# Kernel tuning notes

Measured on AMD Instinct MI355X. Metric: run time of the kernel, lower is better.

The kernel has to match this reference:

```python
import jax, jax.numpy as jnp
import numpy as np

N_TRUCK = 100000
N_CAR = 100000
E = 1600000
H = 128
P = 200000


def _gcn(x, edge_index, edge_weight, W, b, num_nodes):
    """PyG GCNConv: D^{-1/2}(A+I)D^{-1/2} x W + b with self-loop weight 1."""
    h = x @ W  # [N, H]
    row, col = edge_index[0], edge_index[1]
    deg = jax.ops.segment_sum(edge_weight, col, num_segments=num_nodes) + 1.0  # +1 self-loop
    dis = jax.lax.rsqrt(deg)
    norm = dis[row] * edge_weight * dis[col]  # [E]
    agg = jax.ops.segment_sum(norm[:, None] * h[row], col, num_segments=num_nodes)
    agg = agg + (dis * dis)[:, None] * h  # self-loop contribution
    return agg + b


def setup_inputs() -> dict:
    key = jax.random.key(0)
    ks = jax.random.split(key, 12)
    return {
        "x_car": jax.random.normal(ks[0], (N_CAR, 3), dtype=jnp.float32),
        "edge_index_truck": jax.random.randint(ks[1], (2, E), 0, N_TRUCK, dtype=jnp.int64)
        if jax.config.jax_enable_x64 else jax.random.randint(ks[1], (2, E), 0, N_TRUCK, dtype=jnp.int32),
        "edge_index_car": jax.random.randint(ks[2], (2, E), 0, N_CAR, dtype=jnp.int32),
        "edge_weight_car": jax.random.uniform(ks[3], (E,), dtype=jnp.float32),
        "src": jax.random.randint(ks[4], (P,), 0, N_TRUCK + N_CAR, dtype=jnp.int32),
        "dst": jax.random.randint(ks[5], (P,), 0, N_TRUCK + N_CAR, dtype=jnp.int32),
        "n_truck": N_TRUCK,
        "W_truck": jax.random.normal(ks[6], (1, H), dtype=jnp.float32) * 0.5,
        "b_truck": jax.random.normal(ks[7], (H,), dtype=jnp.float32) * 0.1,
        "W_car": jax.random.normal(ks[8], (3, H), dtype=jnp.float32) * 0.5,
        "b_car": jax.random.normal(ks[9], (H,), dtype=jnp.float32) * 0.1,
        "W_lin": jax.random.normal(ks[10], (H, 1), dtype=jnp.float32) * 0.1,
        "b_lin": jax.random.normal(ks[11], (1,), dtype=jnp.float32) * 0.1,
    }


def reference(x_car, edge_index_truck, edge_index_car, edge_weight_car,
              src, dst, n_truck, W_truck, b_truck, W_car, b_car, W_lin, b_lin):
    x_truck_in = jnp.ones((n_truck, 1), dtype=x_car.dtype)
    ew_truck = jnp.ones((edge_index_truck.shape[1],), dtype=x_car.dtype)
    h_truck = _gcn(x_truck_in, edge_index_truck, ew_truck, W_truck, b_truck, n_truck)
    h_car = _gcn(x_car, edge_index_car, edge_weight_car, W_car, b_car, x_car.shape[0])
    x = jnp.concatenate([h_truck, h_car], axis=0)  # [N_truck+N_car, H]
    score = (x[src] * x[dst]) @ W_lin + b_lin  # [P, 1]
    return score
```

## Files before the change

### kernel.cpp

```cpp
#include <hip/hip_runtime.h>

typedef unsigned long long u64;

#define N_TRUCK 100000
#define BLK 256
#define NB 256
#define NPB 391
#define CAP 8192
#define PB 512
#define BLK_PL 512
#define BLK_P 1024
#define CHUNK_MAX 3136
#define ROW_MASK 0x1FFFFu
#define LC_SHIFT 17

#define WS_NEED_NEW 29569920ULL


__global__ __launch_bounds__(BLK_PL, 8)
void k_place(const int* __restrict__ trow, const int* __restrict__ tcol,
             const int* __restrict__ crow, const int* __restrict__ ccol,
             const float* __restrict__ ew, int E_,
             int* __restrict__ curT, int* __restrict__ curC,
             unsigned* __restrict__ pT, u64* __restrict__ pC8,
             const float* __restrict__ Wt, const float* __restrict__ bt,
             const float* __restrict__ Wc, const float* __restrict__ bc,
             const float* __restrict__ wlin, float* __restrict__ G) {
    if (blockIdx.x == PB) {
        int l = threadIdx.x;
        if (l < 64) {
            float acc[21];
#pragma unroll
            for (int k = 0; k < 21; k++) acc[k] = 0.0f;
            for (int h = l; h < 128; h += 64) {
                float m[6] = {Wt[h], bt[h], Wc[h], Wc[128 + h], Wc[256 + h], bc[h]};
                float w = wlin[h];
                int k = 0;
#pragma unroll
                for (int a = 0; a < 6; a++)
#pragma unroll
                    for (int b2 = a; b2 < 6; b2++)
                        acc[k++] += m[a] * m[b2] * w;
            }
            int k = 0;
#pragma unroll
            for (int a = 0; a < 6; a++)
#pragma unroll
                for (int b2 = a; b2 < 6; b2++) {
                    float v = acc[k++];
#pragma unroll
                    for (int off = 32; off; off >>= 1) v += __shfl_down(v, off);
                    if (l == 0) {
                        G[a * 6 + b2] = v;
                        G[b2 * 6 + a] = v;
                    }
                }
        }
        return;
    }

    __shared__ u64 pay8[CHUNK_MAX];
    __shared__ unsigned char bkt[CHUNK_MAX];
    __shared__ int hT[NB], hC[NB];
    __shared__ int shiftA[NB];
    __shared__ int wsum[8];
    unsigned* pay4 = (unsigned*)pay8;

    const int b = blockIdx.x;
    const int t = threadIdx.x;
    const int lane = t & 63, wv = t >> 6;
    const int chunk = (E_ + PB - 1) / PB;
    const int s0 = b * chunk, s1 = min(E_, s0 + chunk);
    const int n = s1 - s0;

    for (int k = t; k < NB; k += BLK_PL) { hT[k] = 0; hC[k] = 0; }
    __syncthreads();
    for (int j = s0 + t; j < s1; j += BLK_PL) {
        int tc = tcol[j];
        int cc = ccol[j];
        atomicAdd(&hT[tc / NPB], 1);
        atomicAdd(&hC[cc / NPB], 1);
    }
    __syncthreads();

    {
        int cntk = 0, inc = 0;
        if (t < NB) {
            cntk = hT[t];
            inc = cntk;
#pragma unroll
            for (int off = 1; off < 64; off <<= 1) {
                int nv = __shfl_up(inc, off);
                if (lane >= off) inc += nv;
            }
            if (lane == 63) wsum[wv] = inc;
        }
        __syncthreads();
        if (t < 4) {
            int pv = wsum[t], pinc = pv;
#pragma unroll
            for (int off = 1; off < 4; off <<= 1) {
                int nv = __shfl_up(pinc, off);
                if (lane >= off) pinc += nv;
            }
            wsum[t] = pinc - pv;
        }
        __syncthreads();
        if (t < NB) {
            int lexcl = (inc - cntk) + wsum[wv];
            int gstart = t * CAP + atomicAdd(&curT[t], cntk);
            hT[t] = lexcl;
            shiftA[t] = gstart - lexcl;
        }
        __syncthreads();
        for (int j = s0 + t; j < s1; j += BLK_PL) {
            int tc = tcol[j];
            int k = tc / NPB;
            int s = atomicAdd(&hT[k], 1);
            pay4[s] = ((unsigned)(tc - k * NPB) << LC_SHIFT) | (unsigned)trow[j];
            bkt[s] = (unsigned char)k;
        }
        __syncthreads();
        for (int s = t; s < n; s += BLK_PL)
            pT[s + shiftA[bkt[s]]] = pay4[s];
        __syncthreads();
    }

    {
        int cntk = 0, inc = 0;
        if (t < NB) {
            cntk = hC[t];
            inc = cntk;
#pragma unroll
            for (int off = 1; off < 64; off <<= 1) {
                int nv = __shfl_up(inc, off);
                if (lane >= off) inc += nv;
            }
            if (lane == 63) wsum[wv] = inc;
        }
        __syncthreads();
        if (t < 4) {
            int pv = wsum[t], pinc = pv;
#pragma unroll
            for (int off = 1; off < 4; off <<= 1) {
                int nv = __shfl_up(pinc, off);
                if (lane >= off) pinc += nv;
            }
            wsum[t] = pinc - pv;
        }
        __syncthreads();
        if (t < NB) {
            int lexcl = (inc - cntk) + wsum[wv];
            int gstart = t * CAP + atomicAdd(&curC[t], cntk);
            hC[t] = lexcl;
            shiftA[t] = gstart - lexcl;
        }
        __syncthreads();
        for (int j = s0 + t; j < s1; j += BLK_PL) {
            int cc = ccol[j];
            int k = cc / NPB;
            int s = atomicAdd(&hC[k], 1);
            unsigned lo = ((unsigned)(cc - k * NPB) << LC_SHIFT) | (unsigned)crow[j];
            pay8[s] = ((u64)__float_as_uint(ew[j]) << 32) | lo;
            bkt[s] = (unsigned char)k;
        }
        __syncthreads();
        for (int s = t; s < n; s += BLK_PL)
            pC8[s + shiftA[bkt[s]]] = pay8[s];
    }
}


__global__ void k_deg2(const unsigned* __restrict__ pT, const u64* __restrict__ pC8,
                       const int* __restrict__ curT, const int* __restrict__ curC,
                       const float* __restrict__ x_car,
                       float* __restrict__ dis_t, float* __restrict__ dis_c,
                       float4* __restrict__ xs4, int nt, int nc) {
    __shared__ float acc[NPB];
    int b = blockIdx.x;
    bool car = b >= NB;
    int bk = car ? b - NB : b;
    int cnt = car ? curC[bk] : curT[bk];
    int s0 = bk * CAP;
    for (int k = threadIdx.x; k < NPB; k += blockDim.x) acc[k] = 0.0f;
    __syncthreads();
    if (car) {
        const ulonglong2* p2 = (const ulonglong2*)(pC8 + s0);
        int half = cnt >> 1;
        for (int j = threadIdx.x; j < half; j += blockDim.x) {
            ulonglong2 v = p2[j];
            atomicAdd(&acc[((unsigned)v.x) >> LC_SHIFT], __uint_as_float((unsigned)(v.x >> 32)));
            atomicAdd(&acc[((unsigned)v.y) >> LC_SHIFT], __uint_as_float((unsigned)(v.y >> 32)));
        }
        if ((cnt & 1) && threadIdx.x == 0) {
            u64 v = pC8[s0 + cnt - 1];
            atomicAdd(&acc[((unsigned)v) >> LC_SHIFT], __uint_as_float((unsigned)(v >> 32)));
        }
    } else {
        const uint2* p2 = (const uint2*)(pT + s0);
        int half = cnt >> 1;
        for (int j = threadIdx.x; j < half; j += blockDim.x) {
            uint2 v = p2[j];
            atomicAdd(&acc[v.x >> LC_SHIFT], 1.0f);
            atomicAdd(&acc[v.y >> LC_SHIFT], 1.0f);
        }
        if ((cnt & 1) && threadIdx.x == 0)
            atomicAdd(&acc[pT[s0 + cnt - 1] >> LC_SHIFT], 1.0f);
    }
    __syncthreads();
    int ntot = car ? nc : nt;
    for (int nn = threadIdx.x; nn < NPB; nn += blockDim.x) {
        int node = bk * NPB + nn;
        if (node < ntot) {
            float d = rsqrtf(acc[nn] + 1.0f);
            if (car) {
                dis_c[node] = d;
                const float* xn = &x_car[3 * node];
                xs4[node] = make_float4(d * xn[0], d * xn[1], d * xn[2], d);
            } else {
                dis_t[node] = d;
            }
        }
    }
}


__global__ void k_agg(const unsigned* __restrict__ pT, const u64* __restrict__ pC8,
                      const int* __restrict__ curT, const int* __restrict__ curC,
                      const float* __restrict__ dis_t, const float* __restrict__ dis_c,
                      const float4* __restrict__ xs4,
                      float* __restrict__ s_t, float4* __restrict__ y4,
                      int nt, int nc) {
    int b = blockIdx.x;
    if (b < NB) {
        __shared__ float sacc[NPB];
        int cnt = curT[b];
        int s0 = b * CAP;
        for (int k = threadIdx.x; k < NPB; k += blockDim.x) sacc[k] = 0.0f;
        __syncthreads();
        const uint2* p2 = (const uint2*)(pT + s0);
        int half = cnt >> 1;
        for (int j = threadIdx.x; j < half; j += blockDim.x) {
            uint2 v = p2[j];
            float da = dis_t[v.x & ROW_MASK];
            float db = dis_t[v.y & ROW_MASK];
            atomicAdd(&sacc[v.x >> LC_SHIFT], da);
            atomicAdd(&sacc[v.y >> LC_SHIFT], db);
        }
        if ((cnt & 1) && threadIdx.x == 0) {
            unsigned v = pT[s0 + cnt - 1];
            atomicAdd(&sacc[v >> LC_SHIFT], dis_t[v & ROW_MASK]);
        }
        __syncthreads();
        for (int nn = threadIdx.x; nn < NPB; nn += blockDim.x) {
            int node = b * NPB + nn;
            if (node < nt) {
                float d = dis_t[node];
                s_t[node] = fmaf(d, sacc[nn], d * d);
            }
        }
    } else {
        int bk = b - NB;
        __shared__ float y[NPB * 5];
        __shared__ float dcl[NPB];
        int cnt = curC[bk];
        int s0 = bk * CAP;
        for (int k = threadIdx.x; k < NPB * 5; k += blockDim.x) y[k] = 0.0f;
        for (int k = threadIdx.x; k < NPB; k += blockDim.x) {
            int node = bk * NPB + k;
            dcl[k] = (node < nc) ? dis_c[node] : 0.0f;
        }
        __syncthreads();
        const ulonglong2* p2 = (const ulonglong2*)(pC8 + s0);
        int half = cnt >> 1;
        for (int j = threadIdx.x; j < half; j += blockDim.x) {
            ulonglong2 v = p2[j];
            unsigned loa = (unsigned)v.x, lob = (unsigned)v.y;
            float4 xa = xs4[loa & ROW_MASK];
            float4 xb = xs4[lob & ROW_MASK];
            int lca = loa >> LC_SHIFT, lcb = lob >> LC_SHIFT;
            float na = __uint_as_float((unsigned)(v.x >> 32)) * dcl[lca];
            float nb = __uint_as_float((unsigned)(v.y >> 32)) * dcl[lcb];
            atomicAdd(&y[lca * 5 + 0], na * xa.x);
            atomicAdd(&y[lca * 5 + 1], na * xa.y);
            atomicAdd(&y[lca * 5 + 2], na * xa.z);
            atomicAdd(&y[lcb * 5 + 0], nb * xb.x);
            atomicAdd(&y[lcb * 5 + 1], nb * xb.y);
            atomicAdd(&y[lcb * 5 + 2], nb * xb.z);
        }
        if ((cnt & 1) && threadIdx.x == 0) {
            u64 v = pC8[s0 + cnt - 1];
            unsigned lo = (unsigned)v;
            float4 xa = xs4[lo & ROW_MASK];
            int lc = lo >> LC_SHIFT;
            float na = __uint_as_float((unsigned)(v >> 32)) * dcl[lc];
            atomicAdd(&y[lc * 5 + 0], na * xa.x);
            atomicAdd(&y[lc * 5 + 1], na * xa.y);
            atomicAdd(&y[lc * 5 + 2], na * xa.z);
        }
        __syncthreads();
        for (int nn = threadIdx.x; nn < NPB; nn += blockDim.x) {
            int node = bk * NPB + nn;
            if (node < nc) {
                float d = dcl[nn];
                float4 xs = xs4[node];
                y4[node] = make_float4(fmaf(d, xs.x, y[nn * 5 + 0]),
                                       fmaf(d, xs.y, y[nn * 5 + 1]),
                                       fmaf(d, xs.z, y[nn * 5 + 2]), 1.0f);
            }
        }
    }
}


__device__ __forceinline__ void load_zf(int i, const float* __restrict__ s_t,
                                        const float4* __restrict__ y4, float z[6]) {
    if (i < N_TRUCK) {
        z[0] = s_t[i]; z[1] = 1.0f; z[2] = 0.0f; z[3] = 0.0f; z[4] = 0.0f; z[5] = 0.0f;
    } else {
        float4 y = y4[i - N_TRUCK];
        z[0] = 0.0f; z[1] = 0.0f; z[2] = y.x; z[3] = y.y; z[4] = y.z; z[5] = 1.0f;
    }
}

__global__ void k_pairs(const int* __restrict__ src, const int* __restrict__ dst, int P_,
                        const float* __restrict__ s_t, const float4* __restrict__ y4,
                        const float* __restrict__ G, const float* __restrict__ b_lin,
                        float* __restrict__ out) {
    int p = blockIdx.x * blockDim.x + threadIdx.x;
    if (p >= P_) return;
    float zs[6], zd[6];
    load_zf(src[p], s_t, y4, zs);
    load_zf(dst[p], s_t, y4, zd);
    float acc = 0.0f;
#pragma unroll
    for (int a = 0; a < 6; a++) {
        float g = 0.0f;
#pragma unroll
        for (int b = 0; b < 6; b++) g = fmaf(G[a * 6 + b], zd[b], g);
        acc = fmaf(zs[a], g, acc);
    }
    out[p] = acc + b_lin[0];
}


__global__ void k_G(const float* __restrict__ Wt, const float* __restrict__ bt,
                    const float* __restrict__ Wc, const float* __restrict__ bc,
                    const float* __restrict__ wlin, float* __restrict__ G) {
    int l = threadIdx.x;
    float acc[21];
#pragma unroll
    for (int k = 0; k < 21; k++) acc[k] = 0.0f;
    for (int h = l; h < 128; h += 64) {
        float m[6] = {Wt[h], bt[h], Wc[h], Wc[128 + h], Wc[256 + h], bc[h]};
        float w = wlin[h];
        int k = 0;
#pragma unroll
        for (int a = 0; a < 6; a++)
#pragma unroll
            for (int b = a; b < 6; b++)
                acc[k++] += m[a] * m[b] * w;
    }
    int k = 0;
#pragma unroll
    for (int a = 0; a < 6; a++)
#pragma unroll
        for (int b = a; b < 6; b++) {
            float v = acc[k++];
#pragma unroll
            for (int off = 32; off; off >>= 1) v += __shfl_down(v, off);
            if (l == 0) {
                G[a * 6 + b] = v;
                G[b * 6 + a] = v;
            }
        }
}

__global__ void k_deg(const int* __restrict__ tcol, const int* __restrict__ ccol,
                      const float* __restrict__ ew, int E_,
                      int* __restrict__ cnt_t, float* __restrict__ degw_c) {
    int i = blockIdx.x * blockDim.x + threadIdx.x;
    if (i >= E_) return;
    atomicAdd(&cnt_t[tcol[i]], 1);
    atomicAdd(&degw_c[ccol[i]], ew[i]);
}

__global__ void k_dis(const int* __restrict__ cnt_t, const float* __restrict__ degw_c,
                      float* __restrict__ dis_t, float* __restrict__ dis_c,
                      int nt, int nc) {
    int i = blockIdx.x * blockDim.x + threadIdx.x;
    if (i < nt) dis_t[i] = rsqrtf((float)cnt_t[i] + 1.0f);
    if (i < nc) dis_c[i] = rsqrtf(degw_c[i] + 1.0f);
}

__global__ void k_scat(const int* __restrict__ trow, const int* __restrict__ tcol,
                       const int* __restrict__ crow, const int* __restrict__ ccol,
                       const float* __restrict__ ew, int E_,
                       const float* __restrict__ dis_t, const float* __restrict__ dis_c,
                       const float* __restrict__ x_car,
                       float* __restrict__ sumdis, float* __restrict__ y4) {
    int i = blockIdx.x * blockDim.x + threadIdx.x;
    if (i >= E_) return;
    atomicAdd(&sumdis[tcol[i]], dis_t[trow[i]]);
    int r = crow[i], c = ccol[i];
    float nrm = dis_c[r] * ew[i] * dis_c[c];
    atomicAdd(&y4[c * 4 + 0], nrm * x_car[r * 3 + 0]);
    atomicAdd(&y4[c * 4 + 1], nrm * x_car[r * 3 + 1]);
    atomicAdd(&y4[c * 4 + 2], nrm * x_car[r * 3 + 2]);
}

__global__ void k_fin(int nt, int nc,
                      const float* __restrict__ dis_t, const float* __restrict__ sumdis,
                      float* __restrict__ s_t,
                      const float* __restrict__ dis_c, const float* __restrict__ x_car,
                      float* __restrict__ y4) {
    int i = blockIdx.x * blockDim.x + threadIdx.x;
    if (i < nt) {
        float d = dis_t[i];
        s_t[i] = d * sumdis[i] + d * d;
    }
    if (i < nc) {
        float d2 = dis_c[i] * dis_c[i];
        y4[i * 4 + 0] += d2 * x_car[i * 3 + 0];
        y4[i * 4 + 1] += d2 * x_car[i * 3 + 1];
        y4[i * 4 + 2] += d2 * x_car[i * 3 + 2];
        y4[i * 4 + 3] = 1.0f;
    }
}


extern "C" void kernel_launch(void* const* d_in, const int* in_sizes, int n_in,
                              void* d_out, int out_size, void* d_ws, size_t ws_size,
                              hipStream_t stream) {
    const float* x_car  = (const float*)d_in[0];
    const int*   ei_t   = (const int*)d_in[1];
    const int*   ei_c   = (const int*)d_in[2];
    const float* ew_c   = (const float*)d_in[3];
    const int*   src    = (const int*)d_in[4];
    const int*   dst    = (const int*)d_in[5];
    const float* W_t    = (const float*)d_in[7];
    const float* b_t    = (const float*)d_in[8];
    const float* W_c    = (const float*)d_in[9];
    const float* b_c    = (const float*)d_in[10];
    const float* W_lin  = (const float*)d_in[11];
    const float* b_lin  = (const float*)d_in[12];
    float* out = (float*)d_out;

    const int NC = in_sizes[0] / 3;
    const int E_ = in_sizes[1] / 2;
    const int P_ = in_sizes[4];

    const int* trow = ei_t;  const int* tcol = ei_t + E_;
    const int* crow = ei_c;  const int* ccol = ei_c + E_;

    char* ws = (char*)d_ws;
    int gP = (P_ + BLK - 1) / BLK;
    int chunk = (E_ + PB - 1) / PB;

    if (ws_size >= WS_NEED_NEW && chunk <= CHUNK_MAX && NB * NPB >= N_TRUCK &&
        NB * NPB >= NC && NB * CAP >= E_ + 8192) {
        int*      curT  = (int*)(ws + 0);
        int*      curC  = (int*)(ws + 1024);
        float*    G     = (float*)(ws + 2048);
        float*    dis_t = (float*)(ws + 4096);
        float*    dis_c = (float*)(ws + 404096);
        float*    s_t   = (float*)(ws + 804096);
        float*    y4    = (float*)(ws + 1204096);
        float4*   xs4   = (float4*)(ws + 2804096);
        unsigned* pT    = (unsigned*)(ws + 4404096);
        u64*      pC8   = (u64*)(ws + 12792704);

        hipMemsetAsync(ws, 0, 2048, stream);
        k_place<<<PB + 1, BLK_PL, 0, stream>>>(trow, tcol, crow, ccol, ew_c, E_,
                                               curT, curC, pT, pC8,
                                               W_t, b_t, W_c, b_c, W_lin, G);
        k_deg2<<<2 * NB, BLK_P, 0, stream>>>(pT, pC8, curT, curC, x_car,
                                             dis_t, dis_c, xs4, N_TRUCK, NC);
        k_agg<<<2 * NB, BLK_P, 0, stream>>>(pT, pC8, curT, curC, dis_t, dis_c,
                                            xs4, s_t, (float4*)y4, N_TRUCK, NC);
        k_pairs<<<gP, BLK, 0, stream>>>(src, dst, P_, s_t, (const float4*)y4, G, b_lin, out);
    } else {
        int*   cnt_t  = (int*)(ws + 0);
        float* sumdis = (float*)(ws + 400000);
        float* degw_c = (float*)(ws + 800000);
        float* y4     = (float*)(ws + 1200000);
        float* dis_t  = (float*)(ws + 2800000);
        float* dis_c  = (float*)(ws + 3200000);
        float* s_t    = (float*)(ws + 3600000);
        float* G      = (float*)(ws + 4000000);

        hipMemsetAsync(ws, 0, 2800000, stream);
        int gE = (E_ + BLK - 1) / BLK;
        int gN = ((N_TRUCK > NC ? N_TRUCK : NC) + BLK - 1) / BLK;
        k_deg<<<gE, BLK, 0, stream>>>(tcol, ccol, ew_c, E_, cnt_t, degw_c);
        k_dis<<<gN, BLK, 0, stream>>>(cnt_t, degw_c, dis_t, dis_c, N_TRUCK, NC);
        k_scat<<<gE, BLK, 0, stream>>>(trow, tcol, crow, ccol, ew_c, E_,
                                       dis_t, dis_c, x_car, sumdis, y4);
        k_fin<<<gN, BLK, 0, stream>>>(N_TRUCK, NC, dis_t, sumdis, s_t, dis_c, x_car, y4);
        k_G<<<1, 64, 0, stream>>>(W_t, b_t, W_c, b_c, W_lin, G);
        k_pairs<<<gP, BLK, 0, stream>>>(src, dst, P_, s_t, (const float4*)y4, G, b_lin, out);
    }
}
```

Measured before the change: 185.4 us.

## Split per-bucket degree and aggregation work across four blocks with reduction passes

Result: slower. 191.3 us (+3.2%).

```diff
diff --git a/kernel.cpp b/kernel.cpp
--- a/kernel.cpp
+++ b/kernel.cpp
@@ -6,15 +6,16 @@
 #define BLK 256
 #define NB 256
 #define NPB 391
+#define NBNPB (NB * NPB)
 #define CAP 8192
 #define PB 512
 #define BLK_PL 512
-#define BLK_P 1024
+#define QS 4
 #define CHUNK_MAX 3136
 #define ROW_MASK 0x1FFFFu
 #define LC_SHIFT 17
 
-#define WS_NEED_NEW 29569920ULL
+#define WS_NEED_NEW 40780672ULL
 
 
 __global__ __launch_bounds__(BLK_PL, 8)
@@ -171,125 +172,94 @@
 }
 
 
-__global__ void k_deg2(const unsigned* __restrict__ pT, const u64* __restrict__ pC8,
-                       const int* __restrict__ curT, const int* __restrict__ curC,
-                       const float* __restrict__ x_car,
-                       float* __restrict__ dis_t, float* __restrict__ dis_c,
-                       float4* __restrict__ xs4, int nt, int nc) {
+__global__ __launch_bounds__(256, 8)
+void k_deg4(const unsigned* __restrict__ pT, const u64* __restrict__ pC8,
+            const int* __restrict__ curT, const int* __restrict__ curC,
+            float* __restrict__ degT4, float* __restrict__ degC4) {
     __shared__ float acc[NPB];
     int b = blockIdx.x;
-    bool car = b >= NB;
-    int bk = car ? b - NB : b;
+    bool car = b >= NB * QS;
+    int bb = car ? b - NB * QS : b;
+    int bk = bb >> 2, q = bb & 3;
     int cnt = car ? curC[bk] : curT[bk];
-    int s0 = bk * CAP;
-    for (int k = threadIdx.x; k < NPB; k += blockDim.x) acc[k] = 0.0f;
+    int qs = (cnt * q) >> 2, qe = (cnt * (q + 1)) >> 2;
+    int base = bk * CAP;
+    int t = threadIdx.x;
+    for (int k = t; k < NPB; k += 256) acc[k] = 0.0f;
     __syncthreads();
     if (car) {
-        const ulonglong2* p2 = (const ulonglong2*)(pC8 + s0);
-        int half = cnt >> 1;
-        for (int j = threadIdx.x; j < half; j += blockDim.x) {
-            ulonglong2 v = p2[j];
-            atomicAdd(&acc[((unsigned)v.x) >> LC_SHIFT], __uint_as_float((unsigned)(v.x >> 32)));
-            atomicAdd(&acc[((unsigned)v.y) >> LC_SHIFT], __uint_as_float((unsigned)(v.y >> 32)));
-        }
-        if ((cnt & 1) && threadIdx.x == 0) {
-            u64 v = pC8[s0 + cnt - 1];
+        for (int j = qs + t; j < qe; j += 256) {
+            u64 v = pC8[base + j];
             atomicAdd(&acc[((unsigned)v) >> LC_SHIFT], __uint_as_float((unsigned)(v >> 32)));
         }
     } else {
-        const uint2* p2 = (const uint2*)(pT + s0);
-        int half = cnt >> 1;
-        for (int j = threadIdx.x; j < half; j += blockDim.x) {
-            uint2 v = p2[j];
-            atomicAdd(&acc[v.x >> LC_SHIFT], 1.0f);
-            atomicAdd(&acc[v.y >> LC_SHIFT], 1.0f);
-        }
-        if ((cnt & 1) && threadIdx.x == 0)
-            atomicAdd(&acc[pT[s0 + cnt - 1] >> LC_SHIFT], 1.0f);
+        for (int j = qs + t; j < qe; j += 256)
+            atomicAdd(&acc[pT[base + j] >> LC_SHIFT], 1.0f);
     }
     __syncthreads();
-    int ntot = car ? nc : nt;
-    for (int nn = threadIdx.x; nn < NPB; nn += blockDim.x) {
-        int node = bk * NPB + nn;
-        if (node < ntot) {
-            float d = rsqrtf(acc[nn] + 1.0f);
-            if (car) {
-                dis_c[node] = d;
-                const float* xn = &x_car[3 * node];
-                xs4[node] = make_float4(d * xn[0], d * xn[1], d * xn[2], d);
-            } else {
-                dis_t[node] = d;
-            }
-        }
-    }
-}
-
-
-__global__ void k_agg(const unsigned* __restrict__ pT, const u64* __restrict__ pC8,
-                      const int* __restrict__ curT, const int* __restrict__ curC,
-                      const float* __restrict__ dis_t, const float* __restrict__ dis_c,
-                      const float4* __restrict__ xs4,
-                      float* __restrict__ s_t, float4* __restrict__ y4,
-                      int nt, int nc) {
+    float* dst = (car ? degC4 : degT4) + q * NBNPB + bk * NPB;
+    for (int nn = t; nn < NPB; nn += 256) dst[nn] = acc[nn];
+}
+
+
+__global__ __launch_bounds__(256, 8)
+void k_fin1(const float* __restrict__ degT4, const float* __restrict__ degC4,
+            const float* __restrict__ x_car,
+            float* __restrict__ dis_t, float* __restrict__ dis_c,
+            float4* __restrict__ xs4, int nt, int nc) {
+    int i = blockIdx.x * 256 + threadIdx.x;
+    if (i < nt)
+        dis_t[i] = rsqrtf(degT4[i] + degT4[NBNPB + i] + degT4[2 * NBNPB + i] +
+                          degT4[3 * NBNPB + i] + 1.0f);
+    if (i < nc) {
+        float d = rsqrtf(degC4[i] + degC4[NBNPB + i] + degC4[2 * NBNPB + i] +
+                         degC4[3 * NBNPB + i] + 1.0f);
+        dis_c[i] = d;
+        const float* xn = &x_car[3 * i];
+        xs4[i] = make_float4(d * xn[0], d * xn[1], d * xn[2], d);
+    }
+}
+
+
+__global__ __launch_bounds__(256, 8)
+void k_agg4(const unsigned* __restrict__ pT, const u64* __restrict__ pC8,
+            const int* __restrict__ curT, const int* __restrict__ curC,
+            const float* __restrict__ dis_t, const float* __restrict__ dis_c,
+            const float4* __restrict__ xs4,
+            float* __restrict__ sum4, float4* __restrict__ yp4, int nc) {
     int b = blockIdx.x;
-    if (b < NB) {
+    int t = threadIdx.x;
+    if (b < NB * QS) {
         __shared__ float sacc[NPB];
-        int cnt = curT[b];
-        int s0 = b * CAP;
-        for (int k = threadIdx.x; k < NPB; k += blockDim.x) sacc[k] = 0.0f;
-        __syncthreads();
-        const uint2* p2 = (const uint2*)(pT + s0);
-        int half = cnt >> 1;
-        for (int j = threadIdx.x; j < half; j += blockDim.x) {
-            uint2 v = p2[j];
-            float da = dis_t[v.x & ROW_MASK];
-            float db = dis_t[v.y & ROW_MASK];
-            atomicAdd(&sacc[v.x >> LC_SHIFT], da);
-            atomicAdd(&sacc[v.y >> LC_SHIFT], db);
-        }
-        if ((cnt & 1) && threadIdx.x == 0) {
-            unsigned v = pT[s0 + cnt - 1];
+        int bk = b >> 2, q = b & 3;
+        int cnt = curT[bk];
+        int qs = (cnt * q) >> 2, qe = (cnt * (q + 1)) >> 2;
+        int base = bk * CAP;
+        for (int k = t; k < NPB; k += 256) sacc[k] = 0.0f;
+        __syncthreads();
+        for (int j = qs + t; j < qe; j += 256) {
+            unsigned v = pT[base + j];
             atomicAdd(&sacc[v >> LC_SHIFT], dis_t[v & ROW_MASK]);
         }
         __syncthreads();
-        for (int nn = threadIdx.x; nn < NPB; nn += blockDim.x) {
-            int node = b * NPB + nn;
-            if (node < nt) {
-                float d = dis_t[node];
-                s_t[node] = fmaf(d, sacc[nn], d * d);
-            }
-        }
+        float* dst = sum4 + q * NBNPB + bk * NPB;
+        for (int nn = t; nn < NPB; nn += 256) dst[nn] = sacc[nn];
     } else {
-        int bk = b - NB;
         __shared__ float y[NPB * 5];
         __shared__ float dcl[NPB];
+        int bb = b - NB * QS;
+        int bk = bb >> 2, q = bb & 3;
         int cnt = curC[bk];
-        int s0 = bk * CAP;
-        for (int k = threadIdx.x; k < NPB * 5; k += blockDim.x) y[k] = 0.0f;
-        for (int k = threadIdx.x; k < NPB; k += blockDim.x) {
+        int qs = (cnt * q) >> 2, qe = (cnt * (q + 1)) >> 2;
+        int base = bk * CAP;
+        for (int k = t; k < NPB * 5; k += 256) y[k] = 0.0f;
+        for (int k = t; k < NPB; k += 256) {
             int node = bk * NPB + k;
             dcl[k] = (node < nc) ? dis_c[node] : 0.0f;
         }
         __syncthreads();
-        const ulonglong2* p2 = (const ulonglong2*)(pC8 + s0);
-        int half = cnt >> 1;
-        for (int j = threadIdx.x; j < half; j += blockDim.x) {
-            ulonglong2 v = p2[j];
-            unsigned loa = (unsigned)v.x, lob = (unsigned)v.y;
-            float4 xa = xs4[loa & ROW_MASK];
-            float4 xb = xs4[lob & ROW_MASK];
-            int lca = loa >> LC_SHIFT, lcb = lob >> LC_SHIFT;
-            float na = __uint_as_float((unsigned)(v.x >> 32)) * dcl[lca];
-            float nb = __uint_as_float((unsigned)(v.y >> 32)) * dcl[lcb];
-            atomicAdd(&y[lca * 5 + 0], na * xa.x);
-            atomicAdd(&y[lca * 5 + 1], na * xa.y);
-            atomicAdd(&y[lca * 5 + 2], na * xa.z);
-            atomicAdd(&y[lcb * 5 + 0], nb * xb.x);
-            atomicAdd(&y[lcb * 5 + 1], nb * xb.y);
-            atomicAdd(&y[lcb * 5 + 2], nb * xb.z);
-        }
-        if ((cnt & 1) && threadIdx.x == 0) {
-            u64 v = pC8[s0 + cnt - 1];
+        for (int j = qs + t; j < qe; j += 256) {
+            u64 v = pC8[base + j];
             unsigned lo = (unsigned)v;
             float4 xa = xs4[lo & ROW_MASK];
             int lc = lo >> LC_SHIFT;
@@ -299,16 +269,32 @@
             atomicAdd(&y[lc * 5 + 2], na * xa.z);
         }
         __syncthreads();
-        for (int nn = threadIdx.x; nn < NPB; nn += blockDim.x) {
-            int node = bk * NPB + nn;
-            if (node < nc) {
-                float d = dcl[nn];
-                float4 xs = xs4[node];
-                y4[node] = make_float4(fmaf(d, xs.x, y[nn * 5 + 0]),
-                                       fmaf(d, xs.y, y[nn * 5 + 1]),
-                                       fmaf(d, xs.z, y[nn * 5 + 2]), 1.0f);
-            }
-        }
+        float4* dst = yp4 + q * NBNPB + bk * NPB;
+        for (int nn = t; nn < NPB; nn += 256)
+            dst[nn] = make_float4(y[nn * 5 + 0], y[nn * 5 + 1], y[nn * 5 + 2], 0.0f);
+    }
+}
+
+
+__global__ __launch_bounds__(256, 8)
+void k_fin2(const float* __restrict__ sum4, const float4* __restrict__ yp4,
+            const float* __restrict__ dis_t, const float* __restrict__ dis_c,
+            const float4* __restrict__ xs4,
+            float* __restrict__ s_t, float4* __restrict__ y4, int nt, int nc) {
+    int i = blockIdx.x * 256 + threadIdx.x;
+    if (i < nt) {
+        float d = dis_t[i];
+        float s = sum4[i] + sum4[NBNPB + i] + sum4[2 * NBNPB + i] + sum4[3 * NBNPB + i];
+        s_t[i] = fmaf(d, s, d * d);
+    }
+    if (i < nc) {
+        float4 a0 = yp4[i], a1 = yp4[NBNPB + i];
+        float4 a2 = yp4[2 * NBNPB + i], a3 = yp4[3 * NBNPB + i];
+        float d = dis_c[i];
+        float4 xs = xs4[i];
+        y4[i] = make_float4(a0.x + a1.x + a2.x + a3.x + d * xs.x,
+                            a0.y + a1.y + a2.y + a3.y + d * xs.y,
+                            a0.z + a1.z + a2.z + a3.z + d * xs.z, 1.0f);
     }
 }
 
@@ -455,6 +441,7 @@
 
     char* ws = (char*)d_ws;
     int gP = (P_ + BLK - 1) / BLK;
+    int gN = (100096 + 255) / 256;
     int chunk = (E_ + PB - 1) / PB;
 
     if (ws_size >= WS_NEED_NEW && chunk <= CHUNK_MAX && NB * NPB >= N_TRUCK &&
@@ -469,15 +456,22 @@
         float4*   xs4   = (float4*)(ws + 2804096);
         unsigned* pT    = (unsigned*)(ws + 4404096);
         u64*      pC8   = (u64*)(ws + 12792704);
+        float*    degT4 = (float*)(ws + 29569920);
+        float*    degC4 = (float*)(ws + 31171456);
+        float*    sum4  = (float*)(ws + 32772992);
+        float4*   yp4   = (float4*)(ws + 34374528);
 
         hipMemsetAsync(ws, 0, 2048, stream);
         k_place<<<PB + 1, BLK_PL, 0, stream>>>(trow, tcol, crow, ccol, ew_c, E_,
                                                curT, curC, pT, pC8,
                                                W_t, b_t, W_c, b_c, W_lin, G);
-        k_deg2<<<2 * NB, BLK_P, 0, stream>>>(pT, pC8, curT, curC, x_car,
-                                             dis_t, dis_c, xs4, N_TRUCK, NC);
-        k_agg<<<2 * NB, BLK_P, 0, stream>>>(pT, pC8, curT, curC, dis_t, dis_c,
-                                            xs4, s_t, (float4*)y4, N_TRUCK, NC);
+        k_deg4<<<2 * NB * QS, 256, 0, stream>>>(pT, pC8, curT, curC, degT4, degC4);
+        k_fin1<<<gN, 256, 0, stream>>>(degT4, degC4, x_car, dis_t, dis_c, xs4,
+                                       N_TRUCK, NC);
+        k_agg4<<<2 * NB * QS, 256, 0, stream>>>(pT, pC8, curT, curC, dis_t, dis_c,
+                                                xs4, sum4, yp4, NC);
+        k_fin2<<<gN, 256, 0, stream>>>(sum4, yp4, dis_t, dis_c, xs4,
+                                       s_t, (float4*)y4, N_TRUCK, NC);
         k_pairs<<<gP, BLK, 0, stream>>>(src, dst, P_, s_t, (const float4*)y4, G, b_lin, out);
     } else {
         int*   cnt_t  = (int*)(ws + 0);
@@ -491,12 +485,12 @@
 
         hipMemsetAsync(ws, 0, 2800000, stream);
         int gE = (E_ + BLK - 1) / BLK;
-        int gN = ((N_TRUCK > NC ? N_TRUCK : NC) + BLK - 1) / BLK;
+        int gN2 = ((N_TRUCK > NC ? N_TRUCK : NC) + BLK - 1) / BLK;
         k_deg<<<gE, BLK, 0, stream>>>(tcol, ccol, ew_c, E_, cnt_t, degw_c);
-        k_dis<<<gN, BLK, 0, stream>>>(cnt_t, degw_c, dis_t, dis_c, N_TRUCK, NC);
+        k_dis<<<gN2, BLK, 0, stream>>>(cnt_t, degw_c, dis_t, dis_c, N_TRUCK, NC);
         k_scat<<<gE, BLK, 0, stream>>>(trow, tcol, crow, ccol, ew_c, E_,
                                        dis_t, dis_c, x_car, sumdis, y4);
-        k_fin<<<gN, BLK, 0, stream>>>(N_TRUCK, NC, dis_t, sumdis, s_t, dis_c, x_car, y4);
+        k_fin<<<gN2, BLK, 0, stream>>>(N_TRUCK, NC, dis_t, sumdis, s_t, dis_c, x_car, y4);
         k_G<<<1, 64, 0, stream>>>(W_t, b_t, W_c, b_c, W_lin, G);
         k_pairs<<<gP, BLK, 0, stream>>>(src, dst, P_, s_t, (const float4*)y4, G, b_lin, out);
     }
```
